# Kernel optimization log

Measured on AMD Instinct MI355X. Metric: run time of the kernel, lower is better.

## Reference

```python
import jax, jax.numpy as jnp
import numpy as np

N = 100000           # nodes
E = 1600000          # directed edges (avg degree 16)
G = 64               # graphs in batch


def gcn_conv(x, src, dst, ew, W, b, n):
    """PyG GCNConv with edge weights and self-loops already appended.

    out[i] = sum_{(j->i)} d[j]^-1/2 * ew * d[i]^-1/2 * (x W)[j] + b
    where d[i] = sum of incoming edge weights at i (incl. self-loop).
    """
    xw = x @ W                                               # [n, out]
    deg = jax.ops.segment_sum(ew, dst, num_segments=n)       # [n]
    dinv = jnp.where(deg > 0, jax.lax.rsqrt(deg), 0.0)
    norm = dinv[src] * ew * dinv[dst]                        # [e]
    msg = xw[src] * norm[:, None]                            # [e, out] gather
    out = jax.ops.segment_sum(msg, dst, num_segments=n)      # scatter-add
    return out + b


def setup_inputs() -> dict:
    key = jax.random.key(0)
    ks = jax.random.split(key, 10)
    x = jax.random.normal(ks[0], (N, 256), dtype=jnp.float32)
    edge_index = jax.random.randint(ks[1], (2, E), 0, N, dtype=jnp.int64)
    edge_weight = jax.random.uniform(ks[2], (E,), dtype=jnp.float32)
    batch = jnp.sort(jax.random.randint(ks[3], (N,), 0, G, dtype=jnp.int64))
    s = 0.05
    W1 = jax.random.normal(ks[4], (256, 128), dtype=jnp.float32) * s
    b1 = jnp.zeros((128,), dtype=jnp.float32)
    W2 = jax.random.normal(ks[5], (128, 64), dtype=jnp.float32) * s
    b2 = jnp.zeros((64,), dtype=jnp.float32)
    Wfc = jax.random.normal(ks[6], (64, 1), dtype=jnp.float32) * s
    bfc = jnp.zeros((1,), dtype=jnp.float32)
    return {"x": x, "edge_index": edge_index, "edge_weight": edge_weight,
            "batch": batch, "W1": W1, "b1": b1, "W2": W2, "b2": b2,
            "Wfc": Wfc, "bfc": bfc}


def reference(x, edge_index, edge_weight, batch, W1, b1, W2, b2, Wfc, bfc):
    n = x.shape[0]
    loop = jnp.arange(n, dtype=edge_index.dtype)
    src = jnp.concatenate([edge_index[0], loop])             # add self-loops
    dst = jnp.concatenate([edge_index[1], loop])
    ew = jnp.concatenate([edge_weight, jnp.ones((n,), x.dtype)])

    h = jax.nn.relu(gcn_conv(x, src, dst, ew, W1, b1, n))    # [N,128]
    h = jax.nn.relu(gcn_conv(h, src, dst, ew, W2, b2, n))    # [N,64]

    # global_mean_pool over batch ids
    sums = jax.ops.segment_sum(h, batch, num_segments=G)     # [G,64]
    cnt = jax.ops.segment_sum(jnp.ones((n,), h.dtype), batch, num_segments=G)
    pooled = sums / jnp.maximum(cnt, 1.0)[:, None]
    return pooled @ Wfc + bfc                                # [G,1]
```

## Files before the change

kernel.cpp:

```cpp
#include <hip/hip_runtime.h>
#include <hip/hip_bf16.h>


static inline int ceil_div_ll(long long a, int b) { return (int)((a + b - 1) / b); }

typedef __attribute__((ext_vector_type(8))) short bf16x8;
typedef __attribute__((ext_vector_type(4))) float f32x4;

#define FIX_SCALE 33554432.0f

__device__ inline unsigned short f2bf(float f) {
    __hip_bfloat16 h = __float2bfloat16(f);
    return *reinterpret_cast<unsigned short*>(&h);
}
__device__ inline float bf2f(unsigned short u) {
    unsigned int x = ((unsigned int)u) << 16;
    return __uint_as_float(x);
}

__global__ void k_init_pk(unsigned long long* __restrict__ pk, int n) {
    int i = blockIdx.x * blockDim.x + threadIdx.x;
    if (i < n) pk[i] = (unsigned long long)(1u << 25);
}

__global__ void k_deg_count(const int* __restrict__ dst, const float* __restrict__ ew,
                            unsigned long long* __restrict__ pk, int* __restrict__ slot, int E) {
    int t = blockIdx.x * blockDim.x + threadIdx.x;
    int e = t * 4;
    if (e + 4 <= E) {
        int4   d4 = *(const int4*)(dst + e);
        float4 w4 = *(const float4*)(ew + e);
        unsigned long long o0 = atomicAdd(&pk[d4.x],
            (1ull << 32) | (unsigned long long)__float2uint_rn(w4.x * FIX_SCALE));
        unsigned long long o1 = atomicAdd(&pk[d4.y],
            (1ull << 32) | (unsigned long long)__float2uint_rn(w4.y * FIX_SCALE));
        unsigned long long o2 = atomicAdd(&pk[d4.z],
            (1ull << 32) | (unsigned long long)__float2uint_rn(w4.z * FIX_SCALE));
        unsigned long long o3 = atomicAdd(&pk[d4.w],
            (1ull << 32) | (unsigned long long)__float2uint_rn(w4.w * FIX_SCALE));
        *(int4*)(slot + e) = make_int4((int)(o0 >> 32), (int)(o1 >> 32),
                                       (int)(o2 >> 32), (int)(o3 >> 32));
    } else if (e < E) {
        for (int k = e; k < E; ++k) {
            unsigned int fx = __float2uint_rn(ew[k] * FIX_SCALE);
            unsigned long long old =
                atomicAdd(&pk[dst[k]], (1ull << 32) | (unsigned long long)fx);
            slot[k] = (int)(old >> 32);
        }
    }
}

__global__ void k_finish(const unsigned long long* __restrict__ pk, float* __restrict__ dinv,
                         int* __restrict__ count, int n) {
    int i = blockIdx.x * blockDim.x + threadIdx.x;
    if (i < n) {
        unsigned long long v = pk[i];
        float deg = (float)(unsigned int)(v & 0xffffffffull) * (1.0f / FIX_SCALE);
        dinv[i] = (deg > 0.f) ? rsqrtf(deg) : 0.f;
        count[i] = (int)(v >> 32);
    }
}

constexpr int SC_T = 256;
constexpr int SC_PER = 16;
constexpr int SC_CHUNK = SC_T * SC_PER;

__global__ void k_scan_a(const int* __restrict__ count, int* __restrict__ bsum, int n) {
    __shared__ int lds[SC_T];
    int b = blockIdx.x, t = threadIdx.x;
    int base = b * SC_CHUNK + t * SC_PER;
    int s = 0;
#pragma unroll
    for (int k = 0; k < SC_PER; ++k) {
        int idx = base + k;
        if (idx < n) s += count[idx];
    }
    lds[t] = s;
    __syncthreads();
    for (int off = 128; off > 0; off >>= 1) {
        if (t < off) lds[t] += lds[t + off];
        __syncthreads();
    }
    if (t == 0) bsum[b] = lds[0];
}

__global__ void k_scan_b(int* __restrict__ bsum, int nb) {
    if (threadIdx.x == 0) {
        int run = 0;
        for (int i = 0; i < nb; ++i) { int c = bsum[i]; bsum[i] = run; run += c; }
    }
}

__global__ void k_scan_c(const int* __restrict__ count, int* __restrict__ rowptr,
                         const int* __restrict__ bsum, int n) {
    __shared__ int lds[SC_T];
    int b = blockIdx.x, t = threadIdx.x;
    int base = b * SC_CHUNK + t * SC_PER;
    int v[SC_PER];
    int s = 0;
#pragma unroll
    for (int k = 0; k < SC_PER; ++k) {
        int idx = base + k;
        v[k] = (idx < n) ? count[idx] : 0;
        s += v[k];
    }
    lds[t] = s;
    for (int off = 1; off < SC_T; off <<= 1) {
        __syncthreads();
        int tmp = (t >= off) ? lds[t - off] : 0;
        __syncthreads();
        lds[t] += tmp;
    }
    __syncthreads();
    int run = bsum[b] + lds[t] - s;
#pragma unroll
    for (int k = 0; k < SC_PER; ++k) {
        int idx = base + k;
        if (idx < n) {
            rowptr[idx] = run;
            run += v[k];
            if (idx == n - 1) rowptr[n] = run;
        }
    }
}

__global__ void k_csr_fill(const int* __restrict__ src, const int* __restrict__ dst,
                           const float* __restrict__ ew, const float* __restrict__ dinv,
                           const int* __restrict__ rowptr, const int* __restrict__ slot,
                           int2* __restrict__ csr, int E) {
    int e = blockIdx.x * blockDim.x + threadIdx.x;
    if (e < E) {
        int s = src[e], d = dst[e];
        int pos = rowptr[d] + slot[e];
        float coef = dinv[s] * ew[e] * dinv[d];
        csr[pos] = make_int2(s, __float_as_int(coef));
    }
}

template <int KDIM, int ODIM>
__global__ void k_wpack(const float* __restrict__ W, unsigned short* __restrict__ wpk) {
    constexpr int NKS = KDIM / 32, NF = ODIM / 16;
    int t = blockIdx.x * blockDim.x + threadIdx.x;
    if (t >= NKS * NF * 64) return;
    int lane = t & 63;
    int nf   = (t >> 6) % NF;
    int ks   = t / (64 * NF);
    int col  = nf * 16 + (lane & 15);
    int kb   = ks * 32 + (lane >> 4) * 8;
    bf16x8 hi, lo;
#pragma unroll
    for (int i = 0; i < 8; ++i) {
        float w = W[(size_t)(kb + i) * ODIM + col];
        unsigned short h = f2bf(w);
        hi[i] = (short)h;
        lo[i] = (short)f2bf(w - bf2f(h));
    }
    size_t base = (size_t)t * 8;
    *(bf16x8*)(wpk + base) = hi;
    *(bf16x8*)(wpk + (size_t)KDIM * ODIM + base) = lo;
}

template <int KDIM, int ODIM>
__global__ void k_gemm_mfma(const float* __restrict__ X,
                            const unsigned short* __restrict__ wpk,
                            unsigned short* __restrict__ Y, int n) {
    constexpr int NKS = KDIM / 32, NF = ODIM / 16;
    int wid  = threadIdx.x >> 6;
    int lane = threadIdx.x & 63;
    int rowbase = blockIdx.x * 64 + wid * 16;
    int arow = rowbase + (lane & 15);
    int kb0  = (lane >> 4) * 8;
    const unsigned short* wlo = wpk + (size_t)KDIM * ODIM;
    bool aok = (arow < n);
    const float* xr = X + (size_t)arow * KDIM + kb0;

    f32x4 acc[NF];
#pragma unroll
    for (int f = 0; f < NF; ++f) acc[f] = (f32x4){0.f, 0.f, 0.f, 0.f};

#pragma unroll
    for (int ks = 0; ks < NKS; ++ks) {
        f32x4 a0 = (f32x4){0.f, 0.f, 0.f, 0.f};
        f32x4 a1 = (f32x4){0.f, 0.f, 0.f, 0.f};
        if (aok) {
            a0 = *(const f32x4*)(xr + ks * 32);
            a1 = *(const f32x4*)(xr + ks * 32 + 4);
        }
        bf16x8 ahi, alo;
#pragma unroll
        for (int i = 0; i < 4; ++i) {
            unsigned short h0 = f2bf(a0[i]);
            ahi[i]     = (short)h0;
            alo[i]     = (short)f2bf(a0[i] - bf2f(h0));
            unsigned short h1 = f2bf(a1[i]);
            ahi[i + 4] = (short)h1;
            alo[i + 4] = (short)f2bf(a1[i] - bf2f(h1));
        }
#pragma unroll
        for (int f = 0; f < NF; ++f) {
            size_t fb = (((size_t)ks * NF + f) * 64 + lane) * 8;
            bf16x8 bhi = *(const bf16x8*)(wpk + fb);
            bf16x8 blo = *(const bf16x8*)(wlo + fb);
            acc[f] = __builtin_amdgcn_mfma_f32_16x16x32_bf16(ahi, bhi, acc[f], 0, 0, 0);
            acc[f] = __builtin_amdgcn_mfma_f32_16x16x32_bf16(alo, bhi, acc[f], 0, 0, 0);
            acc[f] = __builtin_amdgcn_mfma_f32_16x16x32_bf16(ahi, blo, acc[f], 0, 0, 0);
        }
    }

    int r0  = rowbase + (lane >> 4) * 4;
    int col = lane & 15;
#pragma unroll
    for (int f = 0; f < NF; ++f) {
#pragma unroll
        for (int i = 0; i < 4; ++i) {
            int r = r0 + i;
            if (r < n) Y[(size_t)r * ODIM + f * 16 + col] = f2bf(acc[f][i]);
        }
    }
}

template <int KDIM, int ODIM>
__global__ void k_gemm_mfma_bfA(const unsigned short* __restrict__ X,
                                const unsigned short* __restrict__ wpk,
                                unsigned short* __restrict__ Y, int n) {
    constexpr int NKS = KDIM / 32, NF = ODIM / 16;
    int wid  = threadIdx.x >> 6;
    int lane = threadIdx.x & 63;
    int rowbase = blockIdx.x * 64 + wid * 16;
    int arow = rowbase + (lane & 15);
    int kb0  = (lane >> 4) * 8;
    const unsigned short* wlo = wpk + (size_t)KDIM * ODIM;
    bool aok = (arow < n);
    const unsigned short* xr = X + (size_t)arow * KDIM + kb0;

    f32x4 acc[NF];
#pragma unroll
    for (int f = 0; f < NF; ++f) acc[f] = (f32x4){0.f, 0.f, 0.f, 0.f};

#pragma unroll
    for (int ks = 0; ks < NKS; ++ks) {
        bf16x8 a = (bf16x8){0, 0, 0, 0, 0, 0, 0, 0};
        if (aok) a = *(const bf16x8*)(xr + ks * 32);
#pragma unroll
        for (int f = 0; f < NF; ++f) {
            size_t fb = (((size_t)ks * NF + f) * 64 + lane) * 8;
            bf16x8 bhi = *(const bf16x8*)(wpk + fb);
            bf16x8 blo = *(const bf16x8*)(wlo + fb);
            acc[f] = __builtin_amdgcn_mfma_f32_16x16x32_bf16(a, bhi, acc[f], 0, 0, 0);
            acc[f] = __builtin_amdgcn_mfma_f32_16x16x32_bf16(a, blo, acc[f], 0, 0, 0);
        }
    }

    int r0  = rowbase + (lane >> 4) * 4;
    int col = lane & 15;
#pragma unroll
    for (int f = 0; f < NF; ++f) {
#pragma unroll
        for (int i = 0; i < 4; ++i) {
            int r = r0 + i;
            if (r < n) Y[(size_t)r * ODIM + f * 16 + col] = f2bf(acc[f][i]);
        }
    }
}

__global__ void k_gather1(const unsigned short* __restrict__ xw, const int* __restrict__ rowptr,
                          const int2* __restrict__ csr,
                          const float* __restrict__ dinv, const float* __restrict__ bias,
                          unsigned short* __restrict__ out, int n) {
    int wave = threadIdx.x >> 6;
    int lane = threadIdx.x & 63;
    int i = blockIdx.x * 4 + wave;
    if (i >= n) return;

    float dv = dinv[i];
    float sl = dv * dv;
    int e0 = __builtin_amdgcn_readfirstlane(rowptr[i]);
    int e1 = __builtin_amdgcn_readfirstlane(rowptr[i + 1]);

    const unsigned int* base = (const unsigned int*)xw;
    unsigned int su = base[(size_t)i * 64 + lane];
    float ax0 = bf2f((unsigned short)(su & 0xffff)) * sl;
    float ay0 = bf2f((unsigned short)(su >> 16)) * sl;
    float ax1 = 0.f, ay1 = 0.f, ax2 = 0.f, ay2 = 0.f, ax3 = 0.f, ay3 = 0.f;
    int e = e0;
    for (; e + 8 <= e1; e += 8) {
        int2 p0 = csr[e + 0], p1 = csr[e + 1], p2 = csr[e + 2], p3 = csr[e + 3];
        int2 p4 = csr[e + 4], p5 = csr[e + 5], p6 = csr[e + 6], p7 = csr[e + 7];
        unsigned int u0 = base[(size_t)p0.x * 64 + lane];
        unsigned int u1 = base[(size_t)p1.x * 64 + lane];
        unsigned int u2 = base[(size_t)p2.x * 64 + lane];
        unsigned int u3 = base[(size_t)p3.x * 64 + lane];
        unsigned int u4 = base[(size_t)p4.x * 64 + lane];
        unsigned int u5 = base[(size_t)p5.x * 64 + lane];
        unsigned int u6 = base[(size_t)p6.x * 64 + lane];
        unsigned int u7 = base[(size_t)p7.x * 64 + lane];
        float c0 = __int_as_float(p0.y), c1 = __int_as_float(p1.y);
        float c2 = __int_as_float(p2.y), c3 = __int_as_float(p3.y);
        float c4 = __int_as_float(p4.y), c5 = __int_as_float(p5.y);
        float c6 = __int_as_float(p6.y), c7 = __int_as_float(p7.y);
        ax0 += c0 * bf2f((unsigned short)(u0 & 0xffff)); ay0 += c0 * bf2f((unsigned short)(u0 >> 16));
        ax1 += c1 * bf2f((unsigned short)(u1 & 0xffff)); ay1 += c1 * bf2f((unsigned short)(u1 >> 16));
        ax2 += c2 * bf2f((unsigned short)(u2 & 0xffff)); ay2 += c2 * bf2f((unsigned short)(u2 >> 16));
        ax3 += c3 * bf2f((unsigned short)(u3 & 0xffff)); ay3 += c3 * bf2f((unsigned short)(u3 >> 16));
        ax0 += c4 * bf2f((unsigned short)(u4 & 0xffff)); ay0 += c4 * bf2f((unsigned short)(u4 >> 16));
        ax1 += c5 * bf2f((unsigned short)(u5 & 0xffff)); ay1 += c5 * bf2f((unsigned short)(u5 >> 16));
        ax2 += c6 * bf2f((unsigned short)(u6 & 0xffff)); ay2 += c6 * bf2f((unsigned short)(u6 >> 16));
        ax3 += c7 * bf2f((unsigned short)(u7 & 0xffff)); ay3 += c7 * bf2f((unsigned short)(u7 >> 16));
    }
    for (; e + 2 <= e1; e += 2) {
        int2 p0 = csr[e + 0], p1 = csr[e + 1];
        unsigned int u0 = base[(size_t)p0.x * 64 + lane];
        unsigned int u1 = base[(size_t)p1.x * 64 + lane];
        float c0 = __int_as_float(p0.y), c1 = __int_as_float(p1.y);
        ax0 += c0 * bf2f((unsigned short)(u0 & 0xffff)); ay0 += c0 * bf2f((unsigned short)(u0 >> 16));
        ax1 += c1 * bf2f((unsigned short)(u1 & 0xffff)); ay1 += c1 * bf2f((unsigned short)(u1 >> 16));
    }
    if (e < e1) {
        int2 p0 = csr[e];
        unsigned int u0 = base[(size_t)p0.x * 64 + lane];
        float c0 = __int_as_float(p0.y);
        ax0 += c0 * bf2f((unsigned short)(u0 & 0xffff)); ay0 += c0 * bf2f((unsigned short)(u0 >> 16));
    }
    float2 bb = *((const float2*)bias + lane);
    float rx = fmaxf((ax0 + ax1) + (ax2 + ax3) + bb.x, 0.f);
    float ry = fmaxf((ay0 + ay1) + (ay2 + ay3) + bb.y, 0.f);
    unsigned int packed = (unsigned int)f2bf(rx) | ((unsigned int)f2bf(ry) << 16);
    ((unsigned int*)(out + (size_t)i * 128))[lane] = packed;
}

__global__ void k_gather2(const unsigned short* __restrict__ xw, const int* __restrict__ rowptr,
                          const int2* __restrict__ csr,
                          const float* __restrict__ dinv, const float* __restrict__ bias,
                          float* __restrict__ out, int n) {
    int wave = threadIdx.x >> 6;
    int lane = threadIdx.x & 63;
    int i = blockIdx.x * 4 + wave;
    if (i >= n) return;

    float dv = dinv[i];
    float sl = dv * dv;
    int e0 = __builtin_amdgcn_readfirstlane(rowptr[i]);
    int e1 = __builtin_amdgcn_readfirstlane(rowptr[i + 1]);

    float a0 = bf2f(xw[(size_t)i * 64 + lane]) * sl;
    float a1 = 0.f, a2 = 0.f, a3 = 0.f;
    int e = e0;
    for (; e + 8 <= e1; e += 8) {
        int2 p0 = csr[e + 0], p1 = csr[e + 1], p2 = csr[e + 2], p3 = csr[e + 3];
        int2 p4 = csr[e + 4], p5 = csr[e + 5], p6 = csr[e + 6], p7 = csr[e + 7];
        float v0 = bf2f(xw[(size_t)p0.x * 64 + lane]);
        float v1 = bf2f(xw[(size_t)p1.x * 64 + lane]);
        float v2 = bf2f(xw[(size_t)p2.x * 64 + lane]);
        float v3 = bf2f(xw[(size_t)p3.x * 64 + lane]);
        float v4 = bf2f(xw[(size_t)p4.x * 64 + lane]);
        float v5 = bf2f(xw[(size_t)p5.x * 64 + lane]);
        float v6 = bf2f(xw[(size_t)p6.x * 64 + lane]);
        float v7 = bf2f(xw[(size_t)p7.x * 64 + lane]);
        a0 += __int_as_float(p0.y) * v0; a1 += __int_as_float(p1.y) * v1;
        a2 += __int_as_float(p2.y) * v2; a3 += __int_as_float(p3.y) * v3;
        a0 += __int_as_float(p4.y) * v4; a1 += __int_as_float(p5.y) * v5;
        a2 += __int_as_float(p6.y) * v6; a3 += __int_as_float(p7.y) * v7;
    }
    for (; e + 2 <= e1; e += 2) {
        int2 p0 = csr[e + 0], p1 = csr[e + 1];
        a0 += __int_as_float(p0.y) * bf2f(xw[(size_t)p0.x * 64 + lane]);
        a1 += __int_as_float(p1.y) * bf2f(xw[(size_t)p1.x * 64 + lane]);
    }
    if (e < e1) {
        int2 p0 = csr[e];
        a0 += __int_as_float(p0.y) * bf2f(xw[(size_t)p0.x * 64 + lane]);
    }
    float res = fmaxf((a0 + a1) + (a2 + a3) + bias[lane], 0.f);
    out[(size_t)i * 64 + lane] = res;
}

__global__ void k_fill(float* __restrict__ p, int n, float v) {
    int i = blockIdx.x * blockDim.x + threadIdx.x;
    if (i < n) p[i] = v;
}

__global__ void k_pool1(const float* __restrict__ h2, const int* __restrict__ batch,
                        float* __restrict__ sums, int n) {
    int b = blockIdx.x, t = threadIdx.x;
    int chunk = (n + gridDim.x - 1) / gridDim.x;
    int lo = b * chunk, hi = min(lo + chunk, n);
    if (lo >= hi) return;
    int f = t & 63, rg = t >> 6;
    float acc = 0.f;
    int cur = -1;
    for (int r = lo + rg; r < hi; r += 4) {
        int g = batch[r];
        if (g != cur) {
            if (cur >= 0) atomicAdd(&sums[cur * 64 + f], acc);
            acc = 0.f;
            cur = g;
        }
        acc += h2[(size_t)r * 64 + f];
    }
    if (cur >= 0) atomicAdd(&sums[cur * 64 + f], acc);
}

__global__ void k_head(const float* __restrict__ sums, const int* __restrict__ batch,
                       const float* __restrict__ Wfc, const float* __restrict__ bfc,
                       float* __restrict__ out, int n) {
    int g = blockIdx.x;
    int f = threadIdx.x;
    int lo0 = 0, hi0 = n;
    while (lo0 < hi0) { int m = (lo0 + hi0) >> 1; if (batch[m] < g) lo0 = m + 1; else hi0 = m; }
    int lo1 = lo0, hi1 = n;
    while (lo1 < hi1) { int m = (lo1 + hi1) >> 1; if (batch[m] < g + 1) lo1 = m + 1; else hi1 = m; }
    float cnt = (float)(lo1 - lo0);
    float v = sums[g * 64 + f] * Wfc[f];
#pragma unroll
    for (int o = 32; o > 0; o >>= 1) v += __shfl_down(v, o);
    if (f == 0) out[g] = v / fmaxf(cnt, 1.0f) + bfc[0];
}

extern "C" void kernel_launch(void* const* d_in, const int* in_sizes, int n_in,
                              void* d_out, int out_size, void* d_ws, size_t ws_size,
                              hipStream_t stream) {
    const float* x    = (const float*)d_in[0];
    const int*   ei   = (const int*)d_in[1];
    const float* ew   = (const float*)d_in[2];
    const int*   bat  = (const int*)d_in[3];
    const float* W1   = (const float*)d_in[4];
    const float* b1   = (const float*)d_in[5];
    const float* W2   = (const float*)d_in[6];
    const float* b2   = (const float*)d_in[7];
    const float* Wfc  = (const float*)d_in[8];
    const float* bfc  = (const float*)d_in[9];
    float*       out  = (float*)d_out;

    const int N = in_sizes[0] / 256;
    const int E = in_sizes[2];
    const int G = out_size;

    const int* src = ei;
    const int* dst = ei + E;

    const int NB_SCAN = (N + SC_CHUNK - 1) / SC_CHUNK;

    const int Npad = (N + 4) & ~3;
    unsigned long long* pk     = (unsigned long long*)d_ws;
    float*              dinv   = (float*)(pk + Npad);
    int*                count  = (int*)(dinv + Npad);
    int*                rowptr = count + Npad;
    int*                bsum   = rowptr + Npad;
    int*                slot   = bsum + ((NB_SCAN + 4) & ~3);
    int2*               csr    = (int2*)(slot + ((E + 4) & ~3));
    unsigned short*     wpk1   = (unsigned short*)(csr + E);
    unsigned short*     wpk2   = wpk1 + 2 * 256 * 128;
    float*              sums   = (float*)(wpk2 + 2 * 128 * 64);
    unsigned short*     bufA   = (unsigned short*)(sums + ((G * 64 + 4) & ~3));
    unsigned short*     bufH1  = bufA + (size_t)N * 128;
    float*              bufH2  = (float*)(bufH1 + (size_t)N * 128);

    const int B = 256;

    k_init_pk<<<ceil_div_ll(N, B), B, 0, stream>>>(pk, N);
    k_deg_count<<<ceil_div_ll((E + 3) / 4, B), B, 0, stream>>>(dst, ew, pk, slot, E);
    k_finish<<<ceil_div_ll(N, B), B, 0, stream>>>(pk, dinv, count, N);

    k_scan_a<<<NB_SCAN, SC_T, 0, stream>>>(count, bsum, N);
    k_scan_b<<<1, 64, 0, stream>>>(bsum, NB_SCAN);
    k_scan_c<<<NB_SCAN, SC_T, 0, stream>>>(count, rowptr, bsum, N);
    k_csr_fill<<<ceil_div_ll(E, B), B, 0, stream>>>(src, dst, ew, dinv, rowptr,
                                                    slot, csr, E);

    k_wpack<256, 128><<<(8 * 8 * 64 + B - 1) / B, B, 0, stream>>>(W1, wpk1);
    k_wpack<128, 64><<<(4 * 4 * 64 + B - 1) / B, B, 0, stream>>>(W2, wpk2);

    k_gemm_mfma<256, 128><<<ceil_div_ll(N, 64), 256, 0, stream>>>(x, wpk1, bufA, N);
    k_gather1<<<ceil_div_ll(N, 4), 256, 0, stream>>>(
        bufA, rowptr, csr, dinv, b1, bufH1, N);

    k_gemm_mfma_bfA<128, 64><<<ceil_div_ll(N, 64), 256, 0, stream>>>(bufH1, wpk2, bufA, N);
    k_gather2<<<ceil_div_ll(N, 4), 256, 0, stream>>>(
        bufA, rowptr, csr, dinv, b2, bufH2, N);

    k_fill<<<ceil_div_ll(G * 64, B), B, 0, stream>>>(sums, G * 64, 0.0f);
    k_pool1<<<1024, 256, 0, stream>>>(bufH2, bat, sums, N);
    k_head<<<G, 64, 0, stream>>>(sums, bat, Wfc, bfc, out, N);
}
```

Measured before the change: 350.3 us.

## Store layer-1 features in FP8 and fuse layer-2 gather with mean pooling

```diff
diff --git a/kernel.cpp b/kernel.cpp
--- a/kernel.cpp
+++ b/kernel.cpp
@@ -1,5 +1,7 @@
 #include <hip/hip_runtime.h>
 #include <hip/hip_bf16.h>
+#include <hip/hip_fp16.h>
+#include <hip/hip_fp8.h>
 
 
 static inline int ceil_div_ll(long long a, int b) { return (int)((a + b - 1) / b); }
@@ -16,6 +18,18 @@
 __device__ inline float bf2f(unsigned short u) {
     unsigned int x = ((unsigned int)u) << 16;
     return __uint_as_float(x);
+}
+__device__ inline unsigned char f32_to_fp8(float f) {
+    return __hip_cvt_float_to_fp8(f, __HIP_SATFINITE, __HIP_E4M3);
+}
+__device__ inline float fp8_to_f32(unsigned int v) {
+    unsigned int s = v >> 7;
+    unsigned int e = (v >> 3) & 15;
+    unsigned int m = v & 7;
+    float r;
+    if (e) r = __uint_as_float(((e + 120) << 23) | (m << 20));
+    else   r = (float)m * 0.001953125f;
+    return s ? -r : r;
 }
 
 __global__ void k_init_pk(unsigned long long* __restrict__ pk, int n) {
@@ -51,7 +65,7 @@
 }
 
 __global__ void k_finish(const unsigned long long* __restrict__ pk, float* __restrict__ dinv,
-                         int* __restrict__ count, int n) {
+                         int* __restrict__ count, float* __restrict__ sums, int nsums, int n) {
     int i = blockIdx.x * blockDim.x + threadIdx.x;
     if (i < n) {
         unsigned long long v = pk[i];
@@ -59,6 +73,7 @@
         dinv[i] = (deg > 0.f) ? rsqrtf(deg) : 0.f;
         count[i] = (int)(v >> 32);
     }
+    if (i < nsums) sums[i] = 0.0f;
 }
 
 constexpr int SC_T = 256;
@@ -163,7 +178,7 @@
 template <int KDIM, int ODIM>
 __global__ void k_gemm_mfma(const float* __restrict__ X,
                             const unsigned short* __restrict__ wpk,
-                            unsigned short* __restrict__ Y, int n) {
+                            unsigned char* __restrict__ Y, int n) {
     constexpr int NKS = KDIM / 32, NF = ODIM / 16;
     int wid  = threadIdx.x >> 6;
     int lane = threadIdx.x & 63;
@@ -214,7 +229,7 @@
 #pragma unroll
         for (int i = 0; i < 4; ++i) {
             int r = r0 + i;
-            if (r < n) Y[(size_t)r * ODIM + f * 16 + col] = f2bf(acc[f][i]);
+            if (r < n) Y[(size_t)r * ODIM + f * 16 + col] = f32_to_fp8(acc[f][i]);
         }
     }
 }
@@ -263,10 +278,11 @@
     }
 }
 
-__global__ void k_gather1(const unsigned short* __restrict__ xw, const int* __restrict__ rowptr,
-                          const int2* __restrict__ csr,
-                          const float* __restrict__ dinv, const float* __restrict__ bias,
-                          unsigned short* __restrict__ out, int n) {
+__global__ __launch_bounds__(256, 2)
+void k_gather1(const unsigned char* __restrict__ xw, const int* __restrict__ rowptr,
+               const int2* __restrict__ csr,
+               const float* __restrict__ dinv, const float* __restrict__ bias,
+               unsigned short* __restrict__ out, int n) {
     int wave = threadIdx.x >> 6;
     int lane = threadIdx.x & 63;
     int i = blockIdx.x * 4 + wave;
@@ -277,10 +293,10 @@
     int e0 = __builtin_amdgcn_readfirstlane(rowptr[i]);
     int e1 = __builtin_amdgcn_readfirstlane(rowptr[i + 1]);
 
-    const unsigned int* base = (const unsigned int*)xw;
+    const unsigned short* base = (const unsigned short*)xw;
     unsigned int su = base[(size_t)i * 64 + lane];
-    float ax0 = bf2f((unsigned short)(su & 0xffff)) * sl;
-    float ay0 = bf2f((unsigned short)(su >> 16)) * sl;
+    float ax0 = fp8_to_f32(su & 0xff) * sl;
+    float ay0 = fp8_to_f32(su >> 8) * sl;
     float ax1 = 0.f, ay1 = 0.f, ax2 = 0.f, ay2 = 0.f, ax3 = 0.f, ay3 = 0.f;
     int e = e0;
     for (; e + 8 <= e1; e += 8) {
@@ -298,28 +314,28 @@
         float c2 = __int_as_float(p2.y), c3 = __int_as_float(p3.y);
         float c4 = __int_as_float(p4.y), c5 = __int_as_float(p5.y);
         float c6 = __int_as_float(p6.y), c7 = __int_as_float(p7.y);
-        ax0 += c0 * bf2f((unsigned short)(u0 & 0xffff)); ay0 += c0 * bf2f((unsigned short)(u0 >> 16));
-        ax1 += c1 * bf2f((unsigned short)(u1 & 0xffff)); ay1 += c1 * bf2f((unsigned short)(u1 >> 16));
-        ax2 += c2 * bf2f((unsigned short)(u2 & 0xffff)); ay2 += c2 * bf2f((unsigned short)(u2 >> 16));
-        ax3 += c3 * bf2f((unsigned short)(u3 & 0xffff)); ay3 += c3 * bf2f((unsigned short)(u3 >> 16));
-        ax0 += c4 * bf2f((unsigned short)(u4 & 0xffff)); ay0 += c4 * bf2f((unsigned short)(u4 >> 16));
-        ax1 += c5 * bf2f((unsigned short)(u5 & 0xffff)); ay1 += c5 * bf2f((unsigned short)(u5 >> 16));
-        ax2 += c6 * bf2f((unsigned short)(u6 & 0xffff)); ay2 += c6 * bf2f((unsigned short)(u6 >> 16));
-        ax3 += c7 * bf2f((unsigned short)(u7 & 0xffff)); ay3 += c7 * bf2f((unsigned short)(u7 >> 16));
+        ax0 += c0 * fp8_to_f32(u0 & 0xff); ay0 += c0 * fp8_to_f32(u0 >> 8);
+        ax1 += c1 * fp8_to_f32(u1 & 0xff); ay1 += c1 * fp8_to_f32(u1 >> 8);
+        ax2 += c2 * fp8_to_f32(u2 & 0xff); ay2 += c2 * fp8_to_f32(u2 >> 8);
+        ax3 += c3 * fp8_to_f32(u3 & 0xff); ay3 += c3 * fp8_to_f32(u3 >> 8);
+        ax0 += c4 * fp8_to_f32(u4 & 0xff); ay0 += c4 * fp8_to_f32(u4 >> 8);
+        ax1 += c5 * fp8_to_f32(u5 & 0xff); ay1 += c5 * fp8_to_f32(u5 >> 8);
+        ax2 += c6 * fp8_to_f32(u6 & 0xff); ay2 += c6 * fp8_to_f32(u6 >> 8);
+        ax3 += c7 * fp8_to_f32(u7 & 0xff); ay3 += c7 * fp8_to_f32(u7 >> 8);
     }
     for (; e + 2 <= e1; e += 2) {
         int2 p0 = csr[e + 0], p1 = csr[e + 1];
         unsigned int u0 = base[(size_t)p0.x * 64 + lane];
         unsigned int u1 = base[(size_t)p1.x * 64 + lane];
         float c0 = __int_as_float(p0.y), c1 = __int_as_float(p1.y);
-        ax0 += c0 * bf2f((unsigned short)(u0 & 0xffff)); ay0 += c0 * bf2f((unsigned short)(u0 >> 16));
-        ax1 += c1 * bf2f((unsigned short)(u1 & 0xffff)); ay1 += c1 * bf2f((unsigned short)(u1 >> 16));
+        ax0 += c0 * fp8_to_f32(u0 & 0xff); ay0 += c0 * fp8_to_f32(u0 >> 8);
+        ax1 += c1 * fp8_to_f32(u1 & 0xff); ay1 += c1 * fp8_to_f32(u1 >> 8);
     }
     if (e < e1) {
         int2 p0 = csr[e];
         unsigned int u0 = base[(size_t)p0.x * 64 + lane];
         float c0 = __int_as_float(p0.y);
-        ax0 += c0 * bf2f((unsigned short)(u0 & 0xffff)); ay0 += c0 * bf2f((unsigned short)(u0 >> 16));
+        ax0 += c0 * fp8_to_f32(u0 & 0xff); ay0 += c0 * fp8_to_f32(u0 >> 8);
     }
     float2 bb = *((const float2*)bias + lane);
     float rx = fmaxf((ax0 + ax1) + (ax2 + ax3) + bb.x, 0.f);
@@ -328,76 +344,79 @@
     ((unsigned int*)(out + (size_t)i * 128))[lane] = packed;
 }
 
-__global__ void k_gather2(const unsigned short* __restrict__ xw, const int* __restrict__ rowptr,
-                          const int2* __restrict__ csr,
-                          const float* __restrict__ dinv, const float* __restrict__ bias,
-                          float* __restrict__ out, int n) {
+__global__ __launch_bounds__(256, 2)
+void k_gather2_pool(const unsigned short* __restrict__ xw, const int* __restrict__ rowptr,
+                    const int2* __restrict__ csr,
+                    const float* __restrict__ dinv, const float* __restrict__ bias,
+                    const int* __restrict__ batch, float* __restrict__ sums, int n) {
     int wave = threadIdx.x >> 6;
     int lane = threadIdx.x & 63;
     int i = blockIdx.x * 4 + wave;
-    if (i >= n) return;
-
-    float dv = dinv[i];
-    float sl = dv * dv;
-    int e0 = __builtin_amdgcn_readfirstlane(rowptr[i]);
-    int e1 = __builtin_amdgcn_readfirstlane(rowptr[i + 1]);
-
-    float a0 = bf2f(xw[(size_t)i * 64 + lane]) * sl;
-    float a1 = 0.f, a2 = 0.f, a3 = 0.f;
-    int e = e0;
-    for (; e + 8 <= e1; e += 8) {
-        int2 p0 = csr[e + 0], p1 = csr[e + 1], p2 = csr[e + 2], p3 = csr[e + 3];
-        int2 p4 = csr[e + 4], p5 = csr[e + 5], p6 = csr[e + 6], p7 = csr[e + 7];
-        float v0 = bf2f(xw[(size_t)p0.x * 64 + lane]);
-        float v1 = bf2f(xw[(size_t)p1.x * 64 + lane]);
-        float v2 = bf2f(xw[(size_t)p2.x * 64 + lane]);
-        float v3 = bf2f(xw[(size_t)p3.x * 64 + lane]);
-        float v4 = bf2f(xw[(size_t)p4.x * 64 + lane]);
-        float v5 = bf2f(xw[(size_t)p5.x * 64 + lane]);
-        float v6 = bf2f(xw[(size_t)p6.x * 64 + lane]);
-        float v7 = bf2f(xw[(size_t)p7.x * 64 + lane]);
-        a0 += __int_as_float(p0.y) * v0; a1 += __int_as_float(p1.y) * v1;
-        a2 += __int_as_float(p2.y) * v2; a3 += __int_as_float(p3.y) * v3;
-        a0 += __int_as_float(p4.y) * v4; a1 += __int_as_float(p5.y) * v5;
-        a2 += __int_as_float(p6.y) * v6; a3 += __int_as_float(p7.y) * v7;
-    }
-    for (; e + 2 <= e1; e += 2) {
-        int2 p0 = csr[e + 0], p1 = csr[e + 1];
-        a0 += __int_as_float(p0.y) * bf2f(xw[(size_t)p0.x * 64 + lane]);
-        a1 += __int_as_float(p1.y) * bf2f(xw[(size_t)p1.x * 64 + lane]);
-    }
-    if (e < e1) {
-        int2 p0 = csr[e];
-        a0 += __int_as_float(p0.y) * bf2f(xw[(size_t)p0.x * 64 + lane]);
-    }
-    float res = fmaxf((a0 + a1) + (a2 + a3) + bias[lane], 0.f);
-    out[(size_t)i * 64 + lane] = res;
-}
-
-__global__ void k_fill(float* __restrict__ p, int n, float v) {
-    int i = blockIdx.x * blockDim.x + threadIdx.x;
-    if (i < n) p[i] = v;
-}
-
-__global__ void k_pool1(const float* __restrict__ h2, const int* __restrict__ batch,
-                        float* __restrict__ sums, int n) {
-    int b = blockIdx.x, t = threadIdx.x;
-    int chunk = (n + gridDim.x - 1) / gridDim.x;
-    int lo = b * chunk, hi = min(lo + chunk, n);
-    if (lo >= hi) return;
-    int f = t & 63, rg = t >> 6;
-    float acc = 0.f;
-    int cur = -1;
-    for (int r = lo + rg; r < hi; r += 4) {
-        int g = batch[r];
-        if (g != cur) {
-            if (cur >= 0) atomicAdd(&sums[cur * 64 + f], acc);
-            acc = 0.f;
-            cur = g;
-        }
-        acc += h2[(size_t)r * 64 + f];
-    }
-    if (cur >= 0) atomicAdd(&sums[cur * 64 + f], acc);
+    bool valid = (i < n);
+
+    float res = 0.f;
+    int g = -1;
+    if (valid) {
+        float dv = dinv[i];
+        float sl = dv * dv;
+        int e0 = __builtin_amdgcn_readfirstlane(rowptr[i]);
+        int e1 = __builtin_amdgcn_readfirstlane(rowptr[i + 1]);
+
+        float a0 = bf2f(xw[(size_t)i * 64 + lane]) * sl;
+        float a1 = 0.f, a2 = 0.f, a3 = 0.f;
+        int e = e0;
+        for (; e + 8 <= e1; e += 8) {
+            int2 p0 = csr[e + 0], p1 = csr[e + 1], p2 = csr[e + 2], p3 = csr[e + 3];
+            int2 p4 = csr[e + 4], p5 = csr[e + 5], p6 = csr[e + 6], p7 = csr[e + 7];
+            float v0 = bf2f(xw[(size_t)p0.x * 64 + lane]);
+            float v1 = bf2f(xw[(size_t)p1.x * 64 + lane]);
+            float v2 = bf2f(xw[(size_t)p2.x * 64 + lane]);
+            float v3 = bf2f(xw[(size_t)p3.x * 64 + lane]);
+            float v4 = bf2f(xw[(size_t)p4.x * 64 + lane]);
+            float v5 = bf2f(xw[(size_t)p5.x * 64 + lane]);
+            float v6 = bf2f(xw[(size_t)p6.x * 64 + lane]);
+            float v7 = bf2f(xw[(size_t)p7.x * 64 + lane]);
+            a0 += __int_as_float(p0.y) * v0; a1 += __int_as_float(p1.y) * v1;
+            a2 += __int_as_float(p2.y) * v2; a3 += __int_as_float(p3.y) * v3;
+            a0 += __int_as_float(p4.y) * v4; a1 += __int_as_float(p5.y) * v5;
+            a2 += __int_as_float(p6.y) * v6; a3 += __int_as_float(p7.y) * v7;
+        }
+        for (; e + 2 <= e1; e += 2) {
+            int2 p0 = csr[e + 0], p1 = csr[e + 1];
+            a0 += __int_as_float(p0.y) * bf2f(xw[(size_t)p0.x * 64 + lane]);
+            a1 += __int_as_float(p1.y) * bf2f(xw[(size_t)p1.x * 64 + lane]);
+        }
+        if (e < e1) {
+            int2 p0 = csr[e];
+            a0 += __int_as_float(p0.y) * bf2f(xw[(size_t)p0.x * 64 + lane]);
+        }
+        res = fmaxf((a0 + a1) + (a2 + a3) + bias[lane], 0.f);
+        g = batch[i];
+    }
+
+    __shared__ float red[4][64];
+    __shared__ int gid[4];
+    red[wave][lane] = res;
+    if (lane == 0) gid[wave] = g;
+    __syncthreads();
+    if (wave == 0) {
+        float acc = 0.f;
+        int cg = -1;
+        bool has = false;
+#pragma unroll
+        for (int w = 0; w < 4; ++w) {
+            int gw = gid[w];
+            if (gw < 0) continue;
+            if (gw != cg) {
+                if (has) atomicAdd(&sums[cg * 64 + lane], acc);
+                acc = 0.f;
+                cg = gw;
+                has = true;
+            }
+            acc += red[w][lane];
+        }
+        if (has) atomicAdd(&sums[cg * 64 + lane], acc);
+    }
 }
 
 __global__ void k_head(const float* __restrict__ sums, const int* __restrict__ batch,
@@ -451,15 +470,14 @@
     unsigned short*     wpk1   = (unsigned short*)(csr + E);
     unsigned short*     wpk2   = wpk1 + 2 * 256 * 128;
     float*              sums   = (float*)(wpk2 + 2 * 128 * 64);
-    unsigned short*     bufA   = (unsigned short*)(sums + ((G * 64 + 4) & ~3));
-    unsigned short*     bufH1  = bufA + (size_t)N * 128;
-    float*              bufH2  = (float*)(bufH1 + (size_t)N * 128);
+    unsigned char*      bufA   = (unsigned char*)(sums + ((G * 64 + 4) & ~3));
+    unsigned short*     bufH1  = (unsigned short*)(bufA + (size_t)N * 128);
 
     const int B = 256;
 
     k_init_pk<<<ceil_div_ll(N, B), B, 0, stream>>>(pk, N);
     k_deg_count<<<ceil_div_ll((E + 3) / 4, B), B, 0, stream>>>(dst, ew, pk, slot, E);
-    k_finish<<<ceil_div_ll(N, B), B, 0, stream>>>(pk, dinv, count, N);
+    k_finish<<<ceil_div_ll(N, B), B, 0, stream>>>(pk, dinv, count, sums, G * 64, N);
 
     k_scan_a<<<NB_SCAN, SC_T, 0, stream>>>(count, bsum, N);
     k_scan_b<<<1, 64, 0, stream>>>(bsum, NB_SCAN);
@@ -474,11 +492,10 @@
     k_gather1<<<ceil_div_ll(N, 4), 256, 0, stream>>>(
         bufA, rowptr, csr, dinv, b1, bufH1, N);
 
-    k_gemm_mfma_bfA<128, 64><<<ceil_div_ll(N, 64), 256, 0, stream>>>(bufH1, wpk2, bufA, N);
-    k_gather2<<<ceil_div_ll(N, 4), 256, 0, stream>>>(
-        bufA, rowptr, csr, dinv, b2, bufH2, N);
-
-    k_fill<<<ceil_div_ll(G * 64, B), B, 0, stream>>>(sums, G * 64, 0.0f);
-    k_pool1<<<1024, 256, 0, stream>>>(bufH2, bat, sums, N);
+    k_gemm_mfma_bfA<128, 64><<<ceil_div_ll(N, 64), 256, 0, stream>>>(
+        bufH1, wpk2, (unsigned short*)bufA, N);
+    k_gather2_pool<<<ceil_div_ll(N, 4), 256, 0, stream>>>(
+        (const unsigned short*)bufA, rowptr, csr, dinv, b2, bat, sums, N);
+
     k_head<<<G, 64, 0, stream>>>(sums, bat, Wfc, bfc, out, N);
 }
```

After: 364.4 us. +4.0%, slower.
